# Kernel optimization log

Measured on AMD Instinct MI355X. Metric: run time of the kernel, lower is better.

The kernel has to match this reference:

```python
import jax, jax.numpy as jnp
import numpy as np

DIM = 1536
HEADS = 12
HD = DIM // HEADS  # 128
EPS = 1e-6
SINK_SIZE = 1          # frames
MAX_ATTN = 1920        # tokens (sliding window)


def setup_inputs() -> dict:
    key = jax.random.key(0)
    ks = jax.random.split(key, 10)
    B = 1
    F, H, W = 8, 16, 24
    L = F * H * W  # 3072
    s = 0.02
    inp = {
        "x": jax.random.normal(ks[0], (B, L, DIM), jnp.float32),
        "seq_lens": jnp.array([L], jnp.int32),
        "grid_sizes": jnp.array([[F, H, W]], jnp.int32),
        "freqs": jax.random.normal(ks[1], (1024, HD // 2, 2), jnp.float32),
        "wq": jax.random.normal(ks[2], (DIM, DIM), jnp.float32) * s,
        "bq": jnp.zeros((DIM,), jnp.float32),
        "wk": jax.random.normal(ks[3], (DIM, DIM), jnp.float32) * s,
        "bk": jnp.zeros((DIM,), jnp.float32),
        "wv": jax.random.normal(ks[4], (DIM, DIM), jnp.float32) * s,
        "bv": jnp.zeros((DIM,), jnp.float32),
        "wo": jax.random.normal(ks[5], (DIM, DIM), jnp.float32) * s,
        "bo": jnp.zeros((DIM,), jnp.float32),
        "nq_w": jnp.ones((DIM,), jnp.float32),
        "nk_w": jnp.ones((DIM,), jnp.float32),
    }
    return inp


def _rmsnorm(x, w):
    # WanRMSNorm: x * rsqrt(mean(x^2) + eps) * weight
    return x * jax.lax.rsqrt(jnp.mean(x * x, axis=-1, keepdims=True) + EPS) * w


def _rope(x, F, H, W, fc):
    # x: [B, L, n, d]; fc: complex [1024, d//2]
    B, L, n, d = x.shape
    c = d // 2
    c1 = c - 2 * (c // 3)  # temporal split
    c2 = c // 3
    f0, f1, f2 = fc[:, :c1], fc[:, c1:c1 + c2], fc[:, c1 + c2:]
    fr = jnp.concatenate([
        jnp.broadcast_to(f0[:F, None, None, :], (F, H, W, c1)),
        jnp.broadcast_to(f1[None, :H, None, :], (F, H, W, c2)),
        jnp.broadcast_to(f2[None, None, :W, :], (F, H, W, c2)),
    ], axis=-1).reshape(L, 1, c)  # [L, 1, c]
    xp = x.reshape(B, L, n, c, 2)
    xc = jax.lax.complex(xp[..., 0], xp[..., 1])  # [B, L, n, c]
    xr = xc * fr[None]
    return jnp.stack([jnp.real(xr), jnp.imag(xr)], axis=-1).reshape(B, L, n, d)


def reference(x, seq_lens, grid_sizes, freqs, wq, bq, wk, bk, wv, bv, wo, bo, nq_w, nk_w):
    B, L, _ = x.shape
    gs = np.asarray(grid_sizes)[0]
    F, H, W = int(gs[0]), int(gs[1]), int(gs[2])
    fs = H * W  # frame_seqlen
    sink = SINK_SIZE * fs

    q = _rmsnorm(x @ wq.T + bq, nq_w).reshape(B, L, HEADS, HD)
    k = _rmsnorm(x @ wk.T + bk, nk_w).reshape(B, L, HEADS, HD)
    v = (x @ wv.T + bv).reshape(B, L, HEADS, HD)

    fc = jax.lax.complex(freqs[..., 0], freqs[..., 1])  # [1024, HD//2]
    q = _rope(q, F, H, W, fc)
    k = _rope(k, F, H, W, fc)

    # sink + windowed frame-causal block mask (flex_attention block_mask)
    idx = jnp.arange(L)
    qf = idx // fs
    kf = idx // fs
    mask = (kf[None, :] <= qf[:, None]) & (
        (idx[None, :] < sink) | (idx[None, :] >= (qf[:, None] + 1) * fs - MAX_ATTN)
    )  # [L, L]

    scale = 1.0 / np.float32(np.sqrt(HD))
    scores = jnp.einsum('bqnd,bknd->bnqk', q, k) * scale
    scores = jnp.where(mask[None, None], scores, jnp.float32(-1e30))
    attn = jax.nn.softmax(scores, axis=-1)
    out = jnp.einsum('bnqk,bknd->bqnd', attn, v).reshape(B, L, DIM)
    return out @ wo.T + bo
```

## Files before the change

kernel.cpp:

```cpp
#include <hip/hip_runtime.h>
#include <stdint.h>

#define DIMC 1536
#define LTOK 3072
#define HEADS 12
#define HD 128
#define FS 384
#define MAXATTN 1920
#define HTOK 1152
#define NHT 1920

typedef __attribute__((ext_vector_type(4))) float f32x4;
typedef __attribute__((ext_vector_type(8))) short bf16x8;
typedef __attribute__((ext_vector_type(4))) unsigned int u32x4;

__device__ __forceinline__ unsigned short f2bf(float f) {
  union { float f; unsigned int u; } c; c.f = f;
  unsigned int u = c.u + 0x7fffu + ((c.u >> 16) & 1u);
  return (unsigned short)(u >> 16);
}
__device__ __forceinline__ float bf2f(unsigned short s) {
  union { unsigned int u; float f; } c; c.u = (unsigned int)s << 16; return c.f;
}
__device__ __forceinline__ unsigned int cvtpk(float a, float b) {
  unsigned int r;
  asm("v_cvt_pk_bf16_f32 %0, %1, %2" : "=v"(r) : "v"(a), "v"(b));
  return r;
}

__device__ __forceinline__ void dma16(const void* g, void* l) {
  __builtin_amdgcn_global_load_lds(
      (const __attribute__((address_space(1))) unsigned int*)g,
      (__attribute__((address_space(3))) unsigned int*)l, 16, 0, 0);
}

__device__ __forceinline__ int vperm4(int G) {
  return (((G >> 3) & 1) << 3) | (((G >> 1) & 1) << 2) | ((G & 1) << 1) | ((G >> 2) & 1);
}

__global__ __launch_bounds__(256)
void cvt_all_k(const float* __restrict__ x, const float* __restrict__ wq,
               const float* __restrict__ wk, const float* __restrict__ wv,
               const float* __restrict__ wo,
               unsigned short* __restrict__ xb, unsigned short* __restrict__ wqb,
               unsigned short* __restrict__ wkb, unsigned short* __restrict__ wvb,
               unsigned short* __restrict__ wob)
{
  const int i = blockIdx.x * 256 + threadIdx.x;
  const int n0 = LTOK * DIMC / 4;
  const int nw = DIMC * DIMC / 4;
  const float* src; unsigned short* dst; int off;
  if (i < n0) { src = x; dst = xb; off = i; }
  else {
    int j = i - n0; int w = j / nw; off = j - w * nw;
    src = (w == 0) ? wq : (w == 1) ? wk : (w == 2) ? wv : wo;
    dst = (w == 0) ? wqb : (w == 1) ? wkb : (w == 2) ? wvb : wob;
  }
  float4 f = ((const float4*)src)[off];
  uint2 o;
  o.x = (unsigned int)f2bf(f.x) | ((unsigned int)f2bf(f.y) << 16);
  o.y = (unsigned int)f2bf(f.z) | ((unsigned int)f2bf(f.w) << 16);
  ((uint2*)dst)[off] = o;
}

__global__ __launch_bounds__(256)
void gemm_qkv(const unsigned short* __restrict__ A,
              const unsigned short* __restrict__ B0,
              const unsigned short* __restrict__ B1,
              const unsigned short* __restrict__ B2,
              const float* __restrict__ bias0,
              const float* __restrict__ bias1,
              const float* __restrict__ bias2,
              unsigned short* __restrict__ o0, unsigned short* __restrict__ o1,
              unsigned short* __restrict__ vt)
{
  const int f = blockIdx.x;
  const int fp = (f & 7) * 108 + (f >> 3);
  const int z = fp / 288;
  const int rr = fp - z * 288;
  const int by = rr / 12;
  const int bx = rr - by * 12;

  const unsigned short* Bw = (z == 0) ? B0 : (z == 1) ? B1 : B2;
  const float* bias = (z == 0) ? bias0 : (z == 1) ? bias1 : bias2;

  __shared__ __align__(16) unsigned short lA[128 * 64];
  __shared__ __align__(16) unsigned short lB[128 * 64];

  const int tid = threadIdx.x;
  const int wave = tid >> 6;
  const int lane = tid & 63;
  const int m0 = by * 128;
  const int n0 = bx * 128;
  const int wm = (wave >> 1) * 64;
  const int wn = (wave & 1) * 64;

  f32x4 acc[4][4] = {};

  const int srow = tid >> 3;
  const int scol = ((tid & 7) ^ (srow & 7)) * 8;
  const unsigned short* ga = A  + (size_t)(m0 + srow) * DIMC + scol;
  const unsigned short* gb = Bw + (size_t)(n0 + srow) * DIMC + scol;
  unsigned short* la = lA + tid * 8;
  unsigned short* lb = lB + tid * 8;

  const int fr = lane & 15;
  const int g = lane >> 4;
  const int fx = fr & 7;

  for (int k0 = 0; k0 < DIMC; k0 += 64) {
    dma16(ga + k0,                     la);
    dma16(ga + k0 + (size_t)32 * DIMC, la + 2048);
    dma16(ga + k0 + (size_t)64 * DIMC, la + 4096);
    dma16(ga + k0 + (size_t)96 * DIMC, la + 6144);
    dma16(gb + k0,                     lb);
    dma16(gb + k0 + (size_t)32 * DIMC, lb + 2048);
    dma16(gb + k0 + (size_t)64 * DIMC, lb + 4096);
    dma16(gb + k0 + (size_t)96 * DIMC, lb + 6144);
    __syncthreads();

#pragma unroll
    for (int kk = 0; kk < 2; ++kk) {
      const int cx = ((kk * 4 + g) ^ fx) * 8;
      bf16x8 af[4], bf[4];
#pragma unroll
      for (int i = 0; i < 4; ++i)
        af[i] = *(const bf16x8*)&lA[(wm + i * 16 + fr) * 64 + cx];
#pragma unroll
      for (int j = 0; j < 4; ++j)
        bf[j] = *(const bf16x8*)&lB[(wn + j * 16 + fr) * 64 + cx];
#pragma unroll
      for (int i = 0; i < 4; ++i)
#pragma unroll
        for (int j = 0; j < 4; ++j)
          acc[i][j] = __builtin_amdgcn_mfma_f32_16x16x32_bf16(af[i], bf[j], acc[i][j], 0, 0, 0);
    }
    __syncthreads();
  }

  const int col = lane & 15;
  const int rb = (lane >> 4) * 4;
  if (z < 2) {
    unsigned short* outp = z ? o1 : o0;
#pragma unroll
    for (int j = 0; j < 4; ++j) {
      const int gn = n0 + wn + j * 16 + col;
      const float bv = bias[gn];
#pragma unroll
      for (int i = 0; i < 4; ++i)
#pragma unroll
        for (int r = 0; r < 4; ++r) {
          const int gm = m0 + wm + i * 16 + rb + r;
          outp[(size_t)gm * DIMC + gn] = f2bf(acc[i][j][r] + bv);
        }
    }
  } else {
#pragma unroll
    for (int j = 0; j < 4; ++j) {
      const int gn = n0 + wn + j * 16 + col;
      const float bv = bias[gn];
#pragma unroll
      for (int i = 0; i < 4; ++i) {
        const int base = wm + i * 16 + rb;
        const int tile = base & ~63;
        const int toka = m0 + tile + vperm4((base & 63) >> 2) * 4;
        uint2 pk;
        pk.x = (unsigned int)f2bf(acc[i][j][0] + bv) |
               ((unsigned int)f2bf(acc[i][j][1] + bv) << 16);
        pk.y = (unsigned int)f2bf(acc[i][j][2] + bv) |
               ((unsigned int)f2bf(acc[i][j][3] + bv) << 16);
        *(uint2*)(vt + (size_t)gn * LTOK + toka) = pk;
      }
    }
  }
}

__global__ __launch_bounds__(256)
void gemm_wo(const unsigned short* __restrict__ A,
             const unsigned short* __restrict__ Bw,
             const float* __restrict__ bias,
             float* __restrict__ outp)
{
  const int f = blockIdx.x;
  const int fp = (f & 7) * 72 + (f >> 3);
  const int by = fp / 12;
  const int bx = fp - by * 12;

  __shared__ __align__(16) unsigned short lA[64 * 64];
  __shared__ __align__(16) unsigned short lB[128 * 64];

  const int tid = threadIdx.x;
  const int wave = tid >> 6;
  const int lane = tid & 63;
  const int m0 = by * 64;
  const int n0 = bx * 128;
  const int wm = (wave >> 1) * 32;
  const int wn = (wave & 1) * 64;

  f32x4 acc[2][4] = {};

  const int srow = tid >> 3;
  const int scol = ((tid & 7) ^ (srow & 7)) * 8;
  const unsigned short* ga = A  + (size_t)(m0 + srow) * DIMC + scol;
  const unsigned short* gb = Bw + (size_t)(n0 + srow) * DIMC + scol;
  unsigned short* la = lA + tid * 8;
  unsigned short* lb = lB + tid * 8;

  const int fr = lane & 15;
  const int g = lane >> 4;
  const int fx = fr & 7;

  for (int k0 = 0; k0 < DIMC; k0 += 64) {
    dma16(ga + k0,                     la);
    dma16(ga + k0 + (size_t)32 * DIMC, la + 2048);
    dma16(gb + k0,                     lb);
    dma16(gb + k0 + (size_t)32 * DIMC, lb + 2048);
    dma16(gb + k0 + (size_t)64 * DIMC, lb + 4096);
    dma16(gb + k0 + (size_t)96 * DIMC, lb + 6144);
    __syncthreads();

#pragma unroll
    for (int kk = 0; kk < 2; ++kk) {
      const int cx = ((kk * 4 + g) ^ fx) * 8;
      bf16x8 af[2], bf[4];
#pragma unroll
      for (int i = 0; i < 2; ++i)
        af[i] = *(const bf16x8*)&lA[(wm + i * 16 + fr) * 64 + cx];
#pragma unroll
      for (int j = 0; j < 4; ++j)
        bf[j] = *(const bf16x8*)&lB[(wn + j * 16 + fr) * 64 + cx];
#pragma unroll
      for (int i = 0; i < 2; ++i)
#pragma unroll
        for (int j = 0; j < 4; ++j)
          acc[i][j] = __builtin_amdgcn_mfma_f32_16x16x32_bf16(af[i], bf[j], acc[i][j], 0, 0, 0);
    }
    __syncthreads();
  }

  const int col = lane & 15;
  const int rb = (lane >> 4) * 4;
#pragma unroll
  for (int j = 0; j < 4; ++j) {
    const int gn = n0 + wn + j * 16 + col;
    const float bv = bias[gn];
#pragma unroll
    for (int i = 0; i < 2; ++i)
#pragma unroll
      for (int r = 0; r < 4; ++r) {
        const int gm = m0 + wm + i * 16 + rb + r;
        outp[(size_t)gm * DIMC + gn] = acc[i][j][r] + bv;
      }
  }
}

__global__ __launch_bounds__(192)
void post_qkv_k(unsigned short* __restrict__ q, unsigned short* __restrict__ k,
                const float* __restrict__ nqw, const float* __restrict__ nkw,
                const float* __restrict__ freqs)
{
  const int bx = blockIdx.x;
  const int tid = threadIdx.x;
  const int which = bx >= LTOK;
  const int tok = bx - which * LTOK;
  unsigned short* row = (which ? k : q) + (size_t)tok * DIMC;
  const float* nw = which ? nkw : nqw;
  const float sc = which ? 1.f : (0.08838834764831845f * 1.4426950408889634f);
  const int base = tid * 8;

  const bf16x8 rv = *(const bf16x8*)(row + base);
  float vv[8];
  float ss = 0.f;
#pragma unroll
  for (int j = 0; j < 8; ++j) {
    vv[j] = bf2f((unsigned short)rv[j]);
    ss += vv[j] * vv[j];
  }
#pragma unroll
  for (int off = 1; off < 64; off <<= 1) ss += __shfl_xor(ss, off);
  __shared__ float wsum[3];
  if ((tid & 63) == 0) wsum[tid >> 6] = ss;
  __syncthreads();
  const float total = wsum[0] + wsum[1] + wsum[2];
  const float rms = rsqrtf(total * (1.f / DIMC) + 1e-6f);

  const int f = tok / FS;
  const int rem = tok - f * FS;
  const int h = rem / 24;
  const int w = rem - h * 24;

  float nwv[8];
  *(float4*)&nwv[0] = *(const float4*)(nw + base);
  *(float4*)&nwv[4] = *(const float4*)(nw + base + 4);

  u32x4 outp;
#pragma unroll
  for (int pp = 0; pp < 4; ++pp) {
    const int P = (base >> 1) + pp;
    const int p = P & 63;
    const int t = (p < 22) ? f : ((p < 43) ? h : w);
    const float2 fc = *(const float2*)(freqs + t * 128 + p * 2);
    const float e = vv[2 * pp]     * rms * nwv[2 * pp];
    const float o = vv[2 * pp + 1] * rms * nwv[2 * pp + 1];
    outp[pp] = (unsigned int)f2bf((e * fc.x - o * fc.y) * sc) |
               ((unsigned int)f2bf((e * fc.y + o * fc.x) * sc) << 16);
  }
  *(u32x4*)(row + base) = outp;
}

#define KBUF (64 * 128)
#define VBUF (128 * 64)
__global__ __launch_bounds__(512, 4)
void attn_flash(const unsigned short* __restrict__ q,
                const unsigned short* __restrict__ k,
                const unsigned short* __restrict__ vt,
                unsigned short* __restrict__ ab,
                float* __restrict__ Opart,
                float* __restrict__ Opart2,
                float* __restrict__ mlbuf)
{
  const int bid = blockIdx.x;
  int qb, head, chunk, nch;
  if (bid < 36)       { qb = 6 + bid / 12; head = bid % 12; chunk = 0; nch = 1; }
  else if (bid < 108) { int b = bid - 36;  qb = 12 + b / 24; int r = b % 24; head = r >> 1; chunk = r & 1; nch = 2; }
  else if (bid < 432) { int b = bid - 108; qb = 15 + b / 36; int r = b % 36; head = r / 3; chunk = r % 3; nch = 3; }
  else if (bid < 504) { int b = bid - 432; qb = 9 + b / 24;  int r = b % 24; head = r >> 1; chunk = r & 1; nch = 2; }
  else if (bid < 540) { int b = bid - 504; qb = 3 + b / 12; head = b % 12; chunk = 0; nch = 1; }
  else                { int b = bid - 540; qb = b / 12;     head = b % 12; chunk = 0; nch = 1; }

  const int q0 = qb * 128;
  const int qf = qb / 3;
  const int kend = (qf + 1) * FS;
  const int s2 = kend - MAXATTN;
  const bool two = (s2 > FS);
  const int nt1 = (two ? FS : kend) >> 6;
  const int nt  = nt1 + (two ? (MAXATTN >> 6) : 0);
  const int half = nt / nch;
  const int tstart = chunk * half, tend = tstart + half;

  const int tid = threadIdx.x;
  const int wave = tid >> 6, lane = tid & 63;
  const int col = lane & 15;
  const int g = lane >> 4;
  const int g4 = g * 4;

  __shared__ __align__(16) unsigned short Kl[2 * KBUF];
  __shared__ __align__(16) unsigned short Vtl[2 * VBUF];

  bf16x8 qfA[4];
  {
    const unsigned short* qr0 = q + (size_t)(q0 + wave * 16 + col) * DIMC + head * HD;
#pragma unroll
    for (int kk = 0; kk < 4; ++kk)
      qfA[kk] = *(const bf16x8*)(qr0 + kk * 32 + g * 8);
  }

  f32x4 o0[8] = {};
  float m0 = -3.0e38f, l0 = 0.f;

  const int krow = tid >> 4;
  const int kc8  = ((tid & 15) ^ (krow & 15)) * 8;
  const unsigned short* kg = k + (size_t)krow * DIMC + head * HD + kc8;
  const int vrow = tid >> 3;
  const int vc8  = ((tid & 7) ^ (vrow & 7)) * 8;
  const unsigned short* vg = vt + ((size_t)head * HD + vrow) * LTOK + vc8;
  unsigned short* kl = Kl + tid * 8;
  unsigned short* vl = Vtl + tid * 8;

  {
    const int kb = (tstart < nt1) ? tstart * 64 : s2 + (tstart - nt1) * 64;
    const unsigned short* kp = kg + (size_t)kb * DIMC;
    dma16(kp,                     kl);
    dma16(kp + (size_t)32 * DIMC, kl + 32 * 128);
    const unsigned short* vp = vg + kb;
    dma16(vp,                     vl);
    dma16(vp + (size_t)64 * LTOK, vl + 64 * 64);
  }

  for (int t = tstart; t < tend; ++t) {
    const int kcur = ((t - tstart) & 1) * KBUF;
    const int vcur = ((t - tstart) & 1) * VBUF;
    __syncthreads();

    if (t + 1 < tend) {
      const int kb = (t + 1 < nt1) ? (t + 1) * 64 : s2 + (t + 1 - nt1) * 64;
      const int knxt = KBUF - kcur, vnxt = VBUF - vcur;
      const unsigned short* kp = kg + (size_t)kb * DIMC;
      dma16(kp,                     kl + knxt);
      dma16(kp + (size_t)32 * DIMC, kl + knxt + 32 * 128);
      const unsigned short* vp = vg + kb;
      dma16(vp,                     vl + vnxt);
      dma16(vp + (size_t)64 * LTOK, vl + vnxt + 64 * 64);
    }

    f32x4 sA[4] = {};
    __builtin_amdgcn_s_setprio(1);
#pragma unroll
    for (int kt = 0; kt < 4; ++kt) {
      const unsigned short* kr = &Kl[kcur + (kt * 16 + col) * 128];
#pragma unroll
      for (int kk = 0; kk < 4; ++kk) {
        bf16x8 kfr = *(const bf16x8*)(kr + ((kk * 4 + g) ^ col) * 8);
        sA[kt] = __builtin_amdgcn_mfma_f32_16x16x32_bf16(kfr, qfA[kk], sA[kt], 0, 0, 0);
      }
    }
    __builtin_amdgcn_s_setprio(0);

    float mxa = fmaxf(fmaxf(sA[0][0], sA[0][1]), fmaxf(sA[0][2], sA[0][3]));
    float mxb = fmaxf(fmaxf(sA[1][0], sA[1][1]), fmaxf(sA[1][2], sA[1][3]));
    float mxc = fmaxf(fmaxf(sA[2][0], sA[2][1]), fmaxf(sA[2][2], sA[2][3]));
    float mxd = fmaxf(fmaxf(sA[3][0], sA[3][1]), fmaxf(sA[3][2], sA[3][3]));
    float mx = fmaxf(fmaxf(mxa, mxb), fmaxf(mxc, mxd));
    mx = fmaxf(mx, __shfl_xor(mx, 16));
    mx = fmaxf(mx, __shfl_xor(mx, 32));

    if (!__all(mx <= m0 + 8.f)) {
      const float mn = fmaxf(m0, mx);
      const float al = exp2f(m0 - mn);
      m0 = mn;
      l0 *= al;
#pragma unroll
      for (int dt = 0; dt < 8; ++dt) o0[dt] *= al;
    }

    float p[16];
#pragma unroll
    for (int kt = 0; kt < 4; ++kt)
#pragma unroll
      for (int r = 0; r < 4; ++r)
        p[kt * 4 + r] = exp2f(sA[kt][r] - m0);

    float rs = ((p[0] + p[1]) + (p[2] + p[3])) + ((p[4] + p[5]) + (p[6] + p[7]))
             + ((p[8] + p[9]) + (p[10] + p[11])) + ((p[12] + p[13]) + (p[14] + p[15]));
    rs += __shfl_xor(rs, 16);
    rs += __shfl_xor(rs, 32);
    l0 += rs;

    u32x4 tA0, tA1;
    tA0[0] = cvtpk(p[0], p[1]);   tA0[1] = cvtpk(p[2], p[3]);
    tA0[2] = cvtpk(p[4], p[5]);   tA0[3] = cvtpk(p[6], p[7]);
    tA1[0] = cvtpk(p[8], p[9]);   tA1[1] = cvtpk(p[10], p[11]);
    tA1[2] = cvtpk(p[12], p[13]); tA1[3] = cvtpk(p[14], p[15]);
    const bf16x8 pfA0 = __builtin_bit_cast(bf16x8, tA0);
    const bf16x8 pfA1 = __builtin_bit_cast(bf16x8, tA1);

    const int vx0 = (g ^ (col & 7)) * 8;
    const int vx1 = ((4 + g) ^ (col & 7)) * 8;
    __builtin_amdgcn_s_setprio(1);
#pragma unroll
    for (int dt = 0; dt < 8; ++dt) {
      const unsigned short* vr = &Vtl[vcur + (dt * 16 + col) * 64];
      bf16x8 vf0 = *(const bf16x8*)(vr + vx0);
      o0[dt] = __builtin_amdgcn_mfma_f32_16x16x32_bf16(vf0, pfA0, o0[dt], 0, 0, 0);
      bf16x8 vf1 = *(const bf16x8*)(vr + vx1);
      o0[dt] = __builtin_amdgcn_mfma_f32_16x16x32_bf16(vf1, pfA1, o0[dt], 0, 0, 0);
    }
    __builtin_amdgcn_s_setprio(0);
  }

  const int qrow0 = q0 + wave * 16 + col;
  if (nch == 1) {
    const float i0 = 1.f / l0;
    unsigned short* or0 = ab + (size_t)qrow0 * DIMC + head * HD;
#pragma unroll
    for (int dt = 0; dt < 8; ++dt) {
      uint2 pk;
      pk.x = (unsigned int)f2bf(o0[dt][0] * i0) | ((unsigned int)f2bf(o0[dt][1] * i0) << 16);
      pk.y = (unsigned int)f2bf(o0[dt][2] * i0) | ((unsigned int)f2bf(o0[dt][3] * i0) << 16);
      *(uint2*)(or0 + dt * 16 + g4) = pk;
    }
  } else {
    const int tokp0 = qrow0 - HTOK;
    float* ob0;
    if (chunk < 2)
      ob0 = Opart + ((size_t)(chunk * NHT + tokp0) * HEADS + head) * HD;
    else
      ob0 = Opart2 + ((size_t)(tokp0 - 768) * HEADS + head) * HD;
#pragma unroll
    for (int dt = 0; dt < 8; ++dt)
      *(f32x4*)(ob0 + dt * 16 + g4) = o0[dt];
    if (lane < 16) {
      float* mlp0 = mlbuf + 2 * ((size_t)(chunk * NHT + tokp0) * HEADS + head);
      mlp0[0] = m0; mlp0[1] = l0;
    }
  }
}

__global__ __launch_bounds__(384)
void merge_k(const float* __restrict__ Opart, const float* __restrict__ Opart2,
             const float* __restrict__ mlbuf, unsigned short* __restrict__ ab)
{
  const int tokp = blockIdx.x;
  const int tid = threadIdx.x;
  const int e = tid * 4;
  const int head = e >> 7;
  const size_t r0 = (size_t)tokp * DIMC + e;
  float4 o0 = *(const float4*)(Opart + r0);
  float4 o1 = *(const float4*)(Opart + (size_t)NHT * DIMC + r0);
  const float* ml0 = mlbuf + 2 * ((size_t)tokp * HEADS + head);
  const float* ml1 = mlbuf + 2 * ((size_t)(NHT + tokp) * HEADS + head);
  const float m0 = ml0[0], l0 = ml0[1], m1 = ml1[0], l1 = ml1[1];

  const bool three = (tokp >= 768);
  float m2 = -3.0e38f, l2 = 0.f;
  float4 o2 = make_float4(0.f, 0.f, 0.f, 0.f);
  if (three) {
    o2 = *(const float4*)(Opart2 + (size_t)(tokp - 768) * DIMC + e);
    const float* ml2 = mlbuf + 2 * ((size_t)(2 * NHT + tokp) * HEADS + head);
    m2 = ml2[0]; l2 = ml2[1];
  }

  const float mm = fmaxf(fmaxf(m0, m1), m2);
  const float a0 = exp2f(m0 - mm), a1 = exp2f(m1 - mm);
  const float a2 = three ? exp2f(m2 - mm) : 0.f;
  const float inv = 1.f / (l0 * a0 + l1 * a1 + l2 * a2);
  uint2 pk;
  pk.x = (unsigned int)f2bf((o0.x * a0 + o1.x * a1 + o2.x * a2) * inv) |
         ((unsigned int)f2bf((o0.y * a0 + o1.y * a1 + o2.y * a2) * inv) << 16);
  pk.y = (unsigned int)f2bf((o0.z * a0 + o1.z * a1 + o2.z * a2) * inv) |
         ((unsigned int)f2bf((o0.w * a0 + o1.w * a1 + o2.w * a2) * inv) << 16);
  *(uint2*)(ab + (size_t)(HTOK + tokp) * DIMC + e) = pk;
}

extern "C" void kernel_launch(void* const* d_in, const int* in_sizes, int n_in,
                              void* d_out, int out_size, void* d_ws, size_t ws_size,
                              hipStream_t stream)
{
  (void)in_sizes; (void)n_in; (void)out_size; (void)ws_size;
  const float* x     = (const float*)d_in[0];
  const float* freqs = (const float*)d_in[3];
  const float* wq    = (const float*)d_in[4];
  const float* bq    = (const float*)d_in[5];
  const float* wk    = (const float*)d_in[6];
  const float* bk    = (const float*)d_in[7];
  const float* wv    = (const float*)d_in[8];
  const float* bv    = (const float*)d_in[9];
  const float* wo    = (const float*)d_in[10];
  const float* bo    = (const float*)d_in[11];
  const float* nqw   = (const float*)d_in[12];
  const float* nkw   = (const float*)d_in[13];

  char* ws = (char*)d_ws;
  size_t off = 0;
  auto take = [&](size_t bytes) -> void* {
    void* p = ws + off; off += (bytes + 255) & ~(size_t)255; return p;
  };
  unsigned short* wob = (unsigned short*)take((size_t)DIMC * DIMC * 2);
  unsigned short* qb  = (unsigned short*)take((size_t)LTOK * DIMC * 2);
  unsigned short* kb  = (unsigned short*)take((size_t)LTOK * DIMC * 2);
  unsigned short* vb  = (unsigned short*)take((size_t)LTOK * DIMC * 2);
  unsigned short* ab  = (unsigned short*)take((size_t)LTOK * DIMC * 2);
  unsigned short* vtb = (unsigned short*)take((size_t)LTOK * DIMC * 2);
  unsigned short* xb  = (unsigned short*)take((size_t)LTOK * DIMC * 2);
  unsigned short* wqb = (unsigned short*)take((size_t)DIMC * DIMC * 2);
  unsigned short* wkb = (unsigned short*)take((size_t)DIMC * DIMC * 2);
  unsigned short* wvb = (unsigned short*)take((size_t)DIMC * DIMC * 2);
  float* mlb = (float*)take((size_t)3 * NHT * HEADS * 2 * sizeof(float));
  float* Opart  = (float*)xb;
  float* Opart2 = (float*)vb;

  cvt_all_k<<<dim3(13824), dim3(256), 0, stream>>>(x, wq, wk, wv, wo,
                                                   xb, wqb, wkb, wvb, wob);

  gemm_qkv<<<dim3(864), dim3(256), 0, stream>>>(
      xb, wqb, wkb, wvb, bq, bk, bv, qb, kb, vtb);

  post_qkv_k<<<dim3(2 * LTOK), dim3(192), 0, stream>>>(qb, kb, nqw, nkw, freqs);

  attn_flash<<<dim3(576), dim3(512), 0, stream>>>(qb, kb, vtb, ab, Opart, Opart2, mlb);
  merge_k<<<dim3(NHT), dim3(384), 0, stream>>>(Opart, Opart2, mlb, ab);

  gemm_wo<<<dim3(576), dim3(256), 0, stream>>>(
      ab, wob, bo, (float*)d_out);
}
```

Baseline: 279.8 us.

## Split attention per frame into 256-row and 128-row query blocks sharing K/V loads

Re-partitions each frame's 384 query rows into one 256-row block (each wave handles two 16-row tiles) and one 128-row block instead of three 128-row blocks. The paired path reuses each K/V fragment read from LDS for two query tiles and shares a single running max across both tiles. This cuts the attention grid from 576 to 384 blocks and reduces global K/V traffic per query, at the cost of more registers in the paired path, fewer blocks for load balance, and a larger code size from the duplicated loop.

```diff
diff --git a/kernel.cpp b/kernel.cpp
--- a/kernel.cpp
+++ b/kernel.cpp
@@ -320,17 +320,22 @@
                 float* __restrict__ mlbuf)
 {
   const int bid = blockIdx.x;
-  int qb, head, chunk, nch;
-  if (bid < 36)       { qb = 6 + bid / 12; head = bid % 12; chunk = 0; nch = 1; }
-  else if (bid < 108) { int b = bid - 36;  qb = 12 + b / 24; int r = b % 24; head = r >> 1; chunk = r & 1; nch = 2; }
-  else if (bid < 432) { int b = bid - 108; qb = 15 + b / 36; int r = b % 36; head = r / 3; chunk = r % 3; nch = 3; }
-  else if (bid < 504) { int b = bid - 432; qb = 9 + b / 24;  int r = b % 24; head = r >> 1; chunk = r & 1; nch = 2; }
-  else if (bid < 540) { int b = bid - 504; qb = 3 + b / 12; head = b % 12; chunk = 0; nch = 1; }
-  else                { int b = bid - 540; qb = b / 12;     head = b % 12; chunk = 0; nch = 1; }
-
-  const int q0 = qb * 128;
-  const int qf = qb / 3;
-  const int kend = (qf + 1) * FS;
+  int f, head, chunk, nch, pair;
+  if (bid < 12)       { f = 2; head = bid;        chunk = 0; nch = 1; pair = 1; }
+  else if (bid < 36)  { int b = bid - 12;  f = 4; head = b >> 1; chunk = b & 1; nch = 2; pair = 1; }
+  else if (bid < 48)  { f = 1; head = bid - 36;   chunk = 0; nch = 1; pair = 1; }
+  else if (bid < 72)  { int b = bid - 48;  f = 3; head = b >> 1; chunk = b & 1; nch = 2; pair = 1; }
+  else if (bid < 180) { int b = bid - 72;  head = b / 9; int r = b % 9; f = 5 + r / 3; chunk = r % 3; nch = 3; pair = 1; }
+  else if (bid < 192) { f = 2; head = bid - 180;  chunk = 0; nch = 1; pair = 0; }
+  else if (bid < 216) { int b = bid - 192; f = 4; head = b >> 1; chunk = b & 1; nch = 2; pair = 0; }
+  else if (bid < 228) { f = 1; head = bid - 216;  chunk = 0; nch = 1; pair = 0; }
+  else if (bid < 252) { int b = bid - 228; f = 3; head = b >> 1; chunk = b & 1; nch = 2; pair = 0; }
+  else if (bid < 360) { int b = bid - 252; head = b / 9; int r = b % 9; f = 5 + r / 3; chunk = r % 3; nch = 3; pair = 0; }
+  else if (bid < 372) { f = 0; head = bid - 360;  chunk = 0; nch = 1; pair = 1; }
+  else                { f = 0; head = bid - 372;  chunk = 0; nch = 1; pair = 0; }
+
+  const int q0 = f * FS + (pair ? 0 : 256);
+  const int kend = (f + 1) * FS;
   const int s2 = kend - MAXATTN;
   const bool two = (s2 > FS);
   const int nt1 = (two ? FS : kend) >> 6;
@@ -346,17 +351,6 @@
 
   __shared__ __align__(16) unsigned short Kl[2 * KBUF];
   __shared__ __align__(16) unsigned short Vtl[2 * VBUF];
-
-  bf16x8 qfA[4];
-  {
-    const unsigned short* qr0 = q + (size_t)(q0 + wave * 16 + col) * DIMC + head * HD;
-#pragma unroll
-    for (int kk = 0; kk < 4; ++kk)
-      qfA[kk] = *(const bf16x8*)(qr0 + kk * 32 + g * 8);
-  }
-
-  f32x4 o0[8] = {};
-  float m0 = -3.0e38f, l0 = 0.f;
 
   const int krow = tid >> 4;
   const int kc8  = ((tid & 15) ^ (krow & 15)) * 8;
@@ -377,111 +371,273 @@
     dma16(vp + (size_t)64 * LTOK, vl + 64 * 64);
   }
 
-  for (int t = tstart; t < tend; ++t) {
-    const int kcur = ((t - tstart) & 1) * KBUF;
-    const int vcur = ((t - tstart) & 1) * VBUF;
-    __syncthreads();
-
-    if (t + 1 < tend) {
-      const int kb = (t + 1 < nt1) ? (t + 1) * 64 : s2 + (t + 1 - nt1) * 64;
-      const int knxt = KBUF - kcur, vnxt = VBUF - vcur;
-      const unsigned short* kp = kg + (size_t)kb * DIMC;
-      dma16(kp,                     kl + knxt);
-      dma16(kp + (size_t)32 * DIMC, kl + knxt + 32 * 128);
-      const unsigned short* vp = vg + kb;
-      dma16(vp,                     vl + vnxt);
-      dma16(vp + (size_t)64 * LTOK, vl + vnxt + 64 * 64);
-    }
-
-    f32x4 sA[4] = {};
-    __builtin_amdgcn_s_setprio(1);
-#pragma unroll
-    for (int kt = 0; kt < 4; ++kt) {
-      const unsigned short* kr = &Kl[kcur + (kt * 16 + col) * 128];
+  const int vx0 = (g ^ (col & 7)) * 8;
+  const int vx1 = ((4 + g) ^ (col & 7)) * 8;
+
+  if (pair) {
+    bf16x8 qfA[4], qfB[4];
+    {
+      const unsigned short* qr0 = q + (size_t)(q0 + wave * 32 + col) * DIMC + head * HD;
 #pragma unroll
       for (int kk = 0; kk < 4; ++kk) {
-        bf16x8 kfr = *(const bf16x8*)(kr + ((kk * 4 + g) ^ col) * 8);
-        sA[kt] = __builtin_amdgcn_mfma_f32_16x16x32_bf16(kfr, qfA[kk], sA[kt], 0, 0, 0);
-      }
-    }
-    __builtin_amdgcn_s_setprio(0);
-
-    float mxa = fmaxf(fmaxf(sA[0][0], sA[0][1]), fmaxf(sA[0][2], sA[0][3]));
-    float mxb = fmaxf(fmaxf(sA[1][0], sA[1][1]), fmaxf(sA[1][2], sA[1][3]));
-    float mxc = fmaxf(fmaxf(sA[2][0], sA[2][1]), fmaxf(sA[2][2], sA[2][3]));
-    float mxd = fmaxf(fmaxf(sA[3][0], sA[3][1]), fmaxf(sA[3][2], sA[3][3]));
-    float mx = fmaxf(fmaxf(mxa, mxb), fmaxf(mxc, mxd));
-    mx = fmaxf(mx, __shfl_xor(mx, 16));
-    mx = fmaxf(mx, __shfl_xor(mx, 32));
-
-    if (!__all(mx <= m0 + 8.f)) {
-      const float mn = fmaxf(m0, mx);
-      const float al = exp2f(m0 - mn);
-      m0 = mn;
-      l0 *= al;
-#pragma unroll
-      for (int dt = 0; dt < 8; ++dt) o0[dt] *= al;
-    }
-
-    float p[16];
-#pragma unroll
-    for (int kt = 0; kt < 4; ++kt)
-#pragma unroll
-      for (int r = 0; r < 4; ++r)
-        p[kt * 4 + r] = exp2f(sA[kt][r] - m0);
-
-    float rs = ((p[0] + p[1]) + (p[2] + p[3])) + ((p[4] + p[5]) + (p[6] + p[7]))
-             + ((p[8] + p[9]) + (p[10] + p[11])) + ((p[12] + p[13]) + (p[14] + p[15]));
-    rs += __shfl_xor(rs, 16);
-    rs += __shfl_xor(rs, 32);
-    l0 += rs;
-
-    u32x4 tA0, tA1;
-    tA0[0] = cvtpk(p[0], p[1]);   tA0[1] = cvtpk(p[2], p[3]);
-    tA0[2] = cvtpk(p[4], p[5]);   tA0[3] = cvtpk(p[6], p[7]);
-    tA1[0] = cvtpk(p[8], p[9]);   tA1[1] = cvtpk(p[10], p[11]);
-    tA1[2] = cvtpk(p[12], p[13]); tA1[3] = cvtpk(p[14], p[15]);
-    const bf16x8 pfA0 = __builtin_bit_cast(bf16x8, tA0);
-    const bf16x8 pfA1 = __builtin_bit_cast(bf16x8, tA1);
-
-    const int vx0 = (g ^ (col & 7)) * 8;
-    const int vx1 = ((4 + g) ^ (col & 7)) * 8;
-    __builtin_amdgcn_s_setprio(1);
-#pragma unroll
-    for (int dt = 0; dt < 8; ++dt) {
-      const unsigned short* vr = &Vtl[vcur + (dt * 16 + col) * 64];
-      bf16x8 vf0 = *(const bf16x8*)(vr + vx0);
-      o0[dt] = __builtin_amdgcn_mfma_f32_16x16x32_bf16(vf0, pfA0, o0[dt], 0, 0, 0);
-      bf16x8 vf1 = *(const bf16x8*)(vr + vx1);
-      o0[dt] = __builtin_amdgcn_mfma_f32_16x16x32_bf16(vf1, pfA1, o0[dt], 0, 0, 0);
-    }
-    __builtin_amdgcn_s_setprio(0);
-  }
-
-  const int qrow0 = q0 + wave * 16 + col;
-  if (nch == 1) {
-    const float i0 = 1.f / l0;
-    unsigned short* or0 = ab + (size_t)qrow0 * DIMC + head * HD;
-#pragma unroll
-    for (int dt = 0; dt < 8; ++dt) {
-      uint2 pk;
-      pk.x = (unsigned int)f2bf(o0[dt][0] * i0) | ((unsigned int)f2bf(o0[dt][1] * i0) << 16);
-      pk.y = (unsigned int)f2bf(o0[dt][2] * i0) | ((unsigned int)f2bf(o0[dt][3] * i0) << 16);
-      *(uint2*)(or0 + dt * 16 + g4) = pk;
+        qfA[kk] = *(const bf16x8*)(qr0 + kk * 32 + g * 8);
+        qfB[kk] = *(const bf16x8*)(qr0 + (size_t)16 * DIMC + kk * 32 + g * 8);
+      }
+    }
+
+    f32x4 o0[8] = {}, o1[8] = {};
+    float m0 = -3.0e38f, l0 = 0.f, l1 = 0.f;
+
+    for (int t = tstart; t < tend; ++t) {
+      const int kcur = ((t - tstart) & 1) * KBUF;
+      const int vcur = ((t - tstart) & 1) * VBUF;
+      __syncthreads();
+
+      if (t + 1 < tend) {
+        const int kb = (t + 1 < nt1) ? (t + 1) * 64 : s2 + (t + 1 - nt1) * 64;
+        const int knxt = KBUF - kcur, vnxt = VBUF - vcur;
+        const unsigned short* kp = kg + (size_t)kb * DIMC;
+        dma16(kp,                     kl + knxt);
+        dma16(kp + (size_t)32 * DIMC, kl + knxt + 32 * 128);
+        const unsigned short* vp = vg + kb;
+        dma16(vp,                     vl + vnxt);
+        dma16(vp + (size_t)64 * LTOK, vl + vnxt + 64 * 64);
+      }
+
+      f32x4 sA[4] = {}, sB[4] = {};
+      __builtin_amdgcn_s_setprio(1);
+#pragma unroll
+      for (int kt = 0; kt < 4; ++kt) {
+        const unsigned short* kr = &Kl[kcur + (kt * 16 + col) * 128];
+#pragma unroll
+        for (int kk = 0; kk < 4; ++kk) {
+          bf16x8 kfr = *(const bf16x8*)(kr + ((kk * 4 + g) ^ col) * 8);
+          sA[kt] = __builtin_amdgcn_mfma_f32_16x16x32_bf16(kfr, qfA[kk], sA[kt], 0, 0, 0);
+          sB[kt] = __builtin_amdgcn_mfma_f32_16x16x32_bf16(kfr, qfB[kk], sB[kt], 0, 0, 0);
+        }
+      }
+      __builtin_amdgcn_s_setprio(0);
+
+      float a0 = fmaxf(fmaxf(sA[0][0], sA[0][1]), fmaxf(sA[0][2], sA[0][3]));
+      float a1 = fmaxf(fmaxf(sA[1][0], sA[1][1]), fmaxf(sA[1][2], sA[1][3]));
+      float a2 = fmaxf(fmaxf(sA[2][0], sA[2][1]), fmaxf(sA[2][2], sA[2][3]));
+      float a3 = fmaxf(fmaxf(sA[3][0], sA[3][1]), fmaxf(sA[3][2], sA[3][3]));
+      float b0 = fmaxf(fmaxf(sB[0][0], sB[0][1]), fmaxf(sB[0][2], sB[0][3]));
+      float b1 = fmaxf(fmaxf(sB[1][0], sB[1][1]), fmaxf(sB[1][2], sB[1][3]));
+      float b2 = fmaxf(fmaxf(sB[2][0], sB[2][1]), fmaxf(sB[2][2], sB[2][3]));
+      float b3 = fmaxf(fmaxf(sB[3][0], sB[3][1]), fmaxf(sB[3][2], sB[3][3]));
+      float mx = fmaxf(fmaxf(fmaxf(a0, a1), fmaxf(a2, a3)),
+                       fmaxf(fmaxf(b0, b1), fmaxf(b2, b3)));
+      mx = fmaxf(mx, __shfl_xor(mx, 16));
+      mx = fmaxf(mx, __shfl_xor(mx, 32));
+
+      if (!__all(mx <= m0 + 8.f)) {
+        const float mn = fmaxf(m0, mx);
+        const float al = exp2f(m0 - mn);
+        m0 = mn;
+        l0 *= al; l1 *= al;
+#pragma unroll
+        for (int dt = 0; dt < 8; ++dt) { o0[dt] *= al; o1[dt] *= al; }
+      }
+
+      float pa[16], pb[16];
+#pragma unroll
+      for (int kt = 0; kt < 4; ++kt)
+#pragma unroll
+        for (int r = 0; r < 4; ++r) {
+          pa[kt * 4 + r] = exp2f(sA[kt][r] - m0);
+          pb[kt * 4 + r] = exp2f(sB[kt][r] - m0);
+        }
+
+      float rsA = (((pa[0] + pa[1]) + (pa[2] + pa[3])) + ((pa[4] + pa[5]) + (pa[6] + pa[7])))
+                + (((pa[8] + pa[9]) + (pa[10] + pa[11])) + ((pa[12] + pa[13]) + (pa[14] + pa[15])));
+      float rsB = (((pb[0] + pb[1]) + (pb[2] + pb[3])) + ((pb[4] + pb[5]) + (pb[6] + pb[7])))
+                + (((pb[8] + pb[9]) + (pb[10] + pb[11])) + ((pb[12] + pb[13]) + (pb[14] + pb[15])));
+      rsA += __shfl_xor(rsA, 16);
+      rsA += __shfl_xor(rsA, 32);
+      rsB += __shfl_xor(rsB, 16);
+      rsB += __shfl_xor(rsB, 32);
+      l0 += rsA; l1 += rsB;
+
+      u32x4 tA0, tA1, tB0, tB1;
+      tA0[0] = cvtpk(pa[0], pa[1]);   tA0[1] = cvtpk(pa[2], pa[3]);
+      tA0[2] = cvtpk(pa[4], pa[5]);   tA0[3] = cvtpk(pa[6], pa[7]);
+      tA1[0] = cvtpk(pa[8], pa[9]);   tA1[1] = cvtpk(pa[10], pa[11]);
+      tA1[2] = cvtpk(pa[12], pa[13]); tA1[3] = cvtpk(pa[14], pa[15]);
+      tB0[0] = cvtpk(pb[0], pb[1]);   tB0[1] = cvtpk(pb[2], pb[3]);
+      tB0[2] = cvtpk(pb[4], pb[5]);   tB0[3] = cvtpk(pb[6], pb[7]);
+      tB1[0] = cvtpk(pb[8], pb[9]);   tB1[1] = cvtpk(pb[10], pb[11]);
+      tB1[2] = cvtpk(pb[12], pb[13]); tB1[3] = cvtpk(pb[14], pb[15]);
+      const bf16x8 pfA0 = __builtin_bit_cast(bf16x8, tA0);
+      const bf16x8 pfA1 = __builtin_bit_cast(bf16x8, tA1);
+      const bf16x8 pfB0 = __builtin_bit_cast(bf16x8, tB0);
+      const bf16x8 pfB1 = __builtin_bit_cast(bf16x8, tB1);
+
+      __builtin_amdgcn_s_setprio(1);
+#pragma unroll
+      for (int dt = 0; dt < 8; ++dt) {
+        const unsigned short* vr = &Vtl[vcur + (dt * 16 + col) * 64];
+        bf16x8 vf0 = *(const bf16x8*)(vr + vx0);
+        o0[dt] = __builtin_amdgcn_mfma_f32_16x16x32_bf16(vf0, pfA0, o0[dt], 0, 0, 0);
+        o1[dt] = __builtin_amdgcn_mfma_f32_16x16x32_bf16(vf0, pfB0, o1[dt], 0, 0, 0);
+        bf16x8 vf1 = *(const bf16x8*)(vr + vx1);
+        o0[dt] = __builtin_amdgcn_mfma_f32_16x16x32_bf16(vf1, pfA1, o0[dt], 0, 0, 0);
+        o1[dt] = __builtin_amdgcn_mfma_f32_16x16x32_bf16(vf1, pfB1, o1[dt], 0, 0, 0);
+      }
+      __builtin_amdgcn_s_setprio(0);
+    }
+
+    const int qrowA = q0 + wave * 32 + col;
+    if (nch == 1) {
+      const float i0 = 1.f / l0, i1 = 1.f / l1;
+      unsigned short* orA = ab + (size_t)qrowA * DIMC + head * HD;
+      unsigned short* orB = orA + (size_t)16 * DIMC;
+#pragma unroll
+      for (int dt = 0; dt < 8; ++dt) {
+        uint2 pk;
+        pk.x = (unsigned int)f2bf(o0[dt][0] * i0) | ((unsigned int)f2bf(o0[dt][1] * i0) << 16);
+        pk.y = (unsigned int)f2bf(o0[dt][2] * i0) | ((unsigned int)f2bf(o0[dt][3] * i0) << 16);
+        *(uint2*)(orA + dt * 16 + g4) = pk;
+        pk.x = (unsigned int)f2bf(o1[dt][0] * i1) | ((unsigned int)f2bf(o1[dt][1] * i1) << 16);
+        pk.y = (unsigned int)f2bf(o1[dt][2] * i1) | ((unsigned int)f2bf(o1[dt][3] * i1) << 16);
+        *(uint2*)(orB + dt * 16 + g4) = pk;
+      }
+    } else {
+      const int tokp0 = qrowA - HTOK;
+      float* obA;
+      if (chunk < 2)
+        obA = Opart + ((size_t)(chunk * NHT + tokp0) * HEADS + head) * HD;
+      else
+        obA = Opart2 + ((size_t)(tokp0 - 768) * HEADS + head) * HD;
+      float* obB = obA + (size_t)16 * HEADS * HD;
+#pragma unroll
+      for (int dt = 0; dt < 8; ++dt) {
+        *(f32x4*)(obA + dt * 16 + g4) = o0[dt];
+        *(f32x4*)(obB + dt * 16 + g4) = o1[dt];
+      }
+      if (lane < 16) {
+        float* mlpA = mlbuf + 2 * ((size_t)(chunk * NHT + tokp0) * HEADS + head);
+        mlpA[0] = m0; mlpA[1] = l0;
+        float* mlpB = mlpA + 2 * (size_t)16 * HEADS;
+        mlpB[0] = m0; mlpB[1] = l1;
+      }
     }
   } else {
-    const int tokp0 = qrow0 - HTOK;
-    float* ob0;
-    if (chunk < 2)
-      ob0 = Opart + ((size_t)(chunk * NHT + tokp0) * HEADS + head) * HD;
-    else
-      ob0 = Opart2 + ((size_t)(tokp0 - 768) * HEADS + head) * HD;
-#pragma unroll
-    for (int dt = 0; dt < 8; ++dt)
-      *(f32x4*)(ob0 + dt * 16 + g4) = o0[dt];
-    if (lane < 16) {
-      float* mlp0 = mlbuf + 2 * ((size_t)(chunk * NHT + tokp0) * HEADS + head);
-      mlp0[0] = m0; mlp0[1] = l0;
+    bf16x8 qfA[4];
+    {
+      const unsigned short* qr0 = q + (size_t)(q0 + wave * 16 + col) * DIMC + head * HD;
+#pragma unroll
+      for (int kk = 0; kk < 4; ++kk)
+        qfA[kk] = *(const bf16x8*)(qr0 + kk * 32 + g * 8);
+    }
+
+    f32x4 o0[8] = {};
+    float m0 = -3.0e38f, l0 = 0.f;
+
+    for (int t = tstart; t < tend; ++t) {
+      const int kcur = ((t - tstart) & 1) * KBUF;
+      const int vcur = ((t - tstart) & 1) * VBUF;
+      __syncthreads();
+
+      if (t + 1 < tend) {
+        const int kb = (t + 1 < nt1) ? (t + 1) * 64 : s2 + (t + 1 - nt1) * 64;
+        const int knxt = KBUF - kcur, vnxt = VBUF - vcur;
+        const unsigned short* kp = kg + (size_t)kb * DIMC;
+        dma16(kp,                     kl + knxt);
+        dma16(kp + (size_t)32 * DIMC, kl + knxt + 32 * 128);
+        const unsigned short* vp = vg + kb;
+        dma16(vp,                     vl + vnxt);
+        dma16(vp + (size_t)64 * LTOK, vl + vnxt + 64 * 64);
+      }
+
+      f32x4 sA[4] = {};
+      __builtin_amdgcn_s_setprio(1);
+#pragma unroll
+      for (int kt = 0; kt < 4; ++kt) {
+        const unsigned short* kr = &Kl[kcur + (kt * 16 + col) * 128];
+#pragma unroll
+        for (int kk = 0; kk < 4; ++kk) {
+          bf16x8 kfr = *(const bf16x8*)(kr + ((kk * 4 + g) ^ col) * 8);
+          sA[kt] = __builtin_amdgcn_mfma_f32_16x16x32_bf16(kfr, qfA[kk], sA[kt], 0, 0, 0);
+        }
+      }
+      __builtin_amdgcn_s_setprio(0);
+
+      float mxa = fmaxf(fmaxf(sA[0][0], sA[0][1]), fmaxf(sA[0][2], sA[0][3]));
+      float mxb = fmaxf(fmaxf(sA[1][0], sA[1][1]), fmaxf(sA[1][2], sA[1][3]));
+      float mxc = fmaxf(fmaxf(sA[2][0], sA[2][1]), fmaxf(sA[2][2], sA[2][3]));
+      float mxd = fmaxf(fmaxf(sA[3][0], sA[3][1]), fmaxf(sA[3][2], sA[3][3]));
+      float mx = fmaxf(fmaxf(mxa, mxb), fmaxf(mxc, mxd));
+      mx = fmaxf(mx, __shfl_xor(mx, 16));
+      mx = fmaxf(mx, __shfl_xor(mx, 32));
+
+      if (!__all(mx <= m0 + 8.f)) {
+        const float mn = fmaxf(m0, mx);
+        const float al = exp2f(m0 - mn);
+        m0 = mn;
+        l0 *= al;
+#pragma unroll
+        for (int dt = 0; dt < 8; ++dt) o0[dt] *= al;
+      }
+
+      float p[16];
+#pragma unroll
+      for (int kt = 0; kt < 4; ++kt)
+#pragma unroll
+        for (int r = 0; r < 4; ++r)
+          p[kt * 4 + r] = exp2f(sA[kt][r] - m0);
+
+      float rs = ((p[0] + p[1]) + (p[2] + p[3])) + ((p[4] + p[5]) + (p[6] + p[7]))
+               + ((p[8] + p[9]) + (p[10] + p[11])) + ((p[12] + p[13]) + (p[14] + p[15]));
+      rs += __shfl_xor(rs, 16);
+      rs += __shfl_xor(rs, 32);
+      l0 += rs;
+
+      u32x4 tA0, tA1;
+      tA0[0] = cvtpk(p[0], p[1]);   tA0[1] = cvtpk(p[2], p[3]);
+      tA0[2] = cvtpk(p[4], p[5]);   tA0[3] = cvtpk(p[6], p[7]);
+      tA1[0] = cvtpk(p[8], p[9]);   tA1[1] = cvtpk(p[10], p[11]);
+      tA1[2] = cvtpk(p[12], p[13]); tA1[3] = cvtpk(p[14], p[15]);
+      const bf16x8 pfA0 = __builtin_bit_cast(bf16x8, tA0);
+      const bf16x8 pfA1 = __builtin_bit_cast(bf16x8, tA1);
+
+      __builtin_amdgcn_s_setprio(1);
+#pragma unroll
+      for (int dt = 0; dt < 8; ++dt) {
+        const unsigned short* vr = &Vtl[vcur + (dt * 16 + col) * 64];
+        bf16x8 vf0 = *(const bf16x8*)(vr + vx0);
+        o0[dt] = __builtin_amdgcn_mfma_f32_16x16x32_bf16(vf0, pfA0, o0[dt], 0, 0, 0);
+        bf16x8 vf1 = *(const bf16x8*)(vr + vx1);
+        o0[dt] = __builtin_amdgcn_mfma_f32_16x16x32_bf16(vf1, pfA1, o0[dt], 0, 0, 0);
+      }
+      __builtin_amdgcn_s_setprio(0);
+    }
+
+    const int qrow0 = q0 + wave * 16 + col;
+    if (nch == 1) {
+      const float i0 = 1.f / l0;
+      unsigned short* or0 = ab + (size_t)qrow0 * DIMC + head * HD;
+#pragma unroll
+      for (int dt = 0; dt < 8; ++dt) {
+        uint2 pk;
+        pk.x = (unsigned int)f2bf(o0[dt][0] * i0) | ((unsigned int)f2bf(o0[dt][1] * i0) << 16);
+        pk.y = (unsigned int)f2bf(o0[dt][2] * i0) | ((unsigned int)f2bf(o0[dt][3] * i0) << 16);
+        *(uint2*)(or0 + dt * 16 + g4) = pk;
+      }
+    } else {
+      const int tokp0 = qrow0 - HTOK;
+      float* ob0;
+      if (chunk < 2)
+        ob0 = Opart + ((size_t)(chunk * NHT + tokp0) * HEADS + head) * HD;
+      else
+        ob0 = Opart2 + ((size_t)(tokp0 - 768) * HEADS + head) * HD;
+#pragma unroll
+      for (int dt = 0; dt < 8; ++dt)
+        *(f32x4*)(ob0 + dt * 16 + g4) = o0[dt];
+      if (lane < 16) {
+        float* mlp0 = mlbuf + 2 * ((size_t)(chunk * NHT + tokp0) * HEADS + head);
+        mlp0[0] = m0; mlp0[1] = l0;
+      }
     }
   }
 }
@@ -567,7 +723,7 @@
 
   post_qkv_k<<<dim3(2 * LTOK), dim3(192), 0, stream>>>(qb, kb, nqw, nkw, freqs);
 
-  attn_flash<<<dim3(576), dim3(512), 0, stream>>>(qb, kb, vtb, ab, Opart, Opart2, mlb);
+  attn_flash<<<dim3(384), dim3(512), 0, stream>>>(qb, kb, vtb, ab, Opart, Opart2, mlb);
   merge_k<<<dim3(NHT), dim3(384), 0, stream>>>(Opart, Opart2, mlb, ab);
 
   gemm_wo<<<dim3(576), dim3(256), 0, stream>>>(
```

After: 357.8 us. 27.9% more time.
